# Performance work log

Hardware: AMD Instinct MI355X
Metric: run time of the kernel (lower is better)

The kernel has to match this reference:

```python
import jax, jax.numpy as jnp
import numpy as np

N, E = 50000, 800000
IN, MAP, H, O = 256, 64, 4, 64
LEAKY_SLOPE = 0.2


def setup_inputs() -> dict:
    key = jax.random.key(0)
    ks = jax.random.split(key, 12)
    x = jax.random.normal(ks[0], (N, IN), dtype=jnp.float32)
    src = jax.random.randint(ks[1], (E,), 0, N, dtype=jnp.int32)
    dst = jax.random.randint(ks[2], (E,), 0, N, dtype=jnp.int32)
    s = 1.0 / np.sqrt(IN)
    W_gat = jax.random.normal(ks[3], (IN, H * O), dtype=jnp.float32) * s
    attn_l = jax.random.normal(ks[4], (H, O), dtype=jnp.float32) * 0.1
    attn_r = jax.random.normal(ks[5], (H, O), dtype=jnp.float32) * 0.1
    gate_m_W = jax.random.normal(ks[6], (IN, MAP), dtype=jnp.float32) * s
    gate_m_b = jnp.zeros((MAP,), dtype=jnp.float32)
    gate_fn_W = jax.random.normal(ks[7], (2 * IN + MAP, H), dtype=jnp.float32) * (1.0 / np.sqrt(2 * IN + MAP))
    gate_fn_b = jnp.zeros((H,), dtype=jnp.float32)
    merge_W = jax.random.normal(ks[8], (IN + O, O), dtype=jnp.float32) * (1.0 / np.sqrt(IN + O))
    merge_b = jnp.zeros((O,), dtype=jnp.float32)
    return {"x": x, "src": src, "dst": dst, "W_gat": W_gat, "attn_l": attn_l,
            "attn_r": attn_r, "gate_m_W": gate_m_W, "gate_m_b": gate_m_b,
            "gate_fn_W": gate_fn_W, "gate_fn_b": gate_fn_b,
            "merge_W": merge_W, "merge_b": merge_b}


def _forward(x, src, dst, W_gat, attn_l, attn_r, gate_m_W, gate_m_b,
             gate_fn_W, gate_fn_b, merge_W, merge_b):
    n = x.shape[0]
    # --- gate branch: gspmm mean of x, gspmm max of linear_z over in-neighbors ---
    deg = jax.ops.segment_sum(jnp.ones_like(dst, dtype=x.dtype), dst, num_segments=n)
    mean_z = jax.ops.segment_sum(x[src], dst, num_segments=n) / jnp.maximum(deg, 1.0)[:, None]
    z = x @ gate_m_W + gate_m_b  # [N, MAP]
    max_z = jax.ops.segment_max(z[src], dst, num_segments=n)
    max_z = jnp.where(deg[:, None] > 0, max_z, 0.0)  # empty neighborhoods -> 0
    nft = jnp.concatenate([x, max_z, mean_z], axis=1)  # [N, 2*IN+MAP]
    gate = jax.nn.sigmoid(nft @ gate_fn_W + gate_fn_b)  # [N, H]
    # --- GATConv ---
    feat = (x @ W_gat).reshape(n, H, O)  # [N, H, O]
    el = jnp.einsum('nho,ho->nh', feat, attn_l)
    er = jnp.einsum('nho,ho->nh', feat, attn_r)
    e = jax.nn.leaky_relu(el[src] + er[dst], negative_slope=LEAKY_SLOPE)  # [E, H]
    m = jax.ops.segment_max(e, dst, num_segments=n)  # [N, H]
    m = jnp.where(jnp.isfinite(m), m, 0.0)
    ex = jnp.exp(e - m[dst])  # [E, H]
    s = jax.ops.segment_sum(ex, dst, num_segments=n)  # [N, H]
    alpha = ex / jnp.maximum(s[dst], 1e-16)  # [E, H]
    attn_out = jax.ops.segment_sum(feat[src] * alpha[:, :, None], dst, num_segments=n)  # [N, H, O]
    # --- gated merge ---
    gated = (gate[:, :, None] * attn_out).mean(axis=1)  # [N, O]
    merge = jnp.concatenate([x, gated], axis=1) @ merge_W + merge_b  # [N, O]
    return merge


def reference(x, src, dst, W_gat, attn_l, attn_r, gate_m_W, gate_m_b,
              gate_fn_W, gate_fn_b, merge_W, merge_b):
    return _forward(x, src, dst, W_gat, attn_l, attn_r, gate_m_W, gate_m_b,
                    gate_fn_W, gate_fn_b, merge_W, merge_b)
```

## Files before the change

kernel.cpp:

```cpp
#include <hip/hip_runtime.h>
#include <math.h>

#define NN 50000
#define NE 800000
#define LEAKY 0.2f
#define NT 26
#define CAP 96
#define NBT (8 * NT * 64)
#define BT_BLKS 54
#define GEMM_BLKS 782
#define SCAT_BLKS 3125
#define FUSE_BLKS 3907

typedef short bf16x8 __attribute__((ext_vector_type(8)));
typedef float f32x4 __attribute__((ext_vector_type(4)));
typedef float f32x2 __attribute__((ext_vector_type(2)));

__device__ __forceinline__ unsigned short f2bf(float f) {
  unsigned u = __float_as_uint(f);
  u += 0x7fffu + ((u >> 16) & 1u);
  return (unsigned short)(u >> 16);
}
__device__ __forceinline__ float leaky(float v) { return v > 0.0f ? v : LEAKY * v; }
__device__ __forceinline__ float rlf(float v, int l) {
  return __uint_as_float(__builtin_amdgcn_readlane(__float_as_uint(v), l));
}
__device__ __forceinline__ int rli(int v, int l) {
  return __builtin_amdgcn_readlane(v, l);
}

__device__ __forceinline__ bf16x8 ld_a_bf16(const float* p) {
  float4 fa = *(const float4*)p;
  float4 fb = *(const float4*)(p + 4);
  unsigned r0, r1, r2, r3;
  asm("v_cvt_pk_bf16_f32 %0, %1, %2" : "=v"(r0) : "v"(fa.x), "v"(fa.y));
  asm("v_cvt_pk_bf16_f32 %0, %1, %2" : "=v"(r1) : "v"(fa.z), "v"(fa.w));
  asm("v_cvt_pk_bf16_f32 %0, %1, %2" : "=v"(r2) : "v"(fb.x), "v"(fb.y));
  asm("v_cvt_pk_bf16_f32 %0, %1, %2" : "=v"(r3) : "v"(fb.z), "v"(fb.w));
  union { uint4 u; bf16x8 v; } c;
  c.u = make_uint4(r0, r1, r2, r3);
  return c.v;
}

#if defined(__has_builtin)
#if __has_builtin(__builtin_amdgcn_cvt_pk_f32_fp8) && \
    __has_builtin(__builtin_amdgcn_cvt_pk_fp8_f32) && \
    __has_builtin(__builtin_amdgcn_cvt_f32_fp8)
#define FP8_HW 1
#endif
#endif

#ifdef FP8_HW
__device__ __forceinline__ unsigned char f2fp8(float v) {
  return (unsigned char)(__builtin_amdgcn_cvt_pk_fp8_f32(v, v, 0u, false) & 0xFF);
}
__device__ __forceinline__ f32x2 fp8x2_lo(unsigned int v) {
  return __builtin_amdgcn_cvt_pk_f32_fp8(v, false);
}
__device__ __forceinline__ f32x2 fp8x2_hi(unsigned int v) {
  return __builtin_amdgcn_cvt_pk_f32_fp8(v, true);
}
__device__ __forceinline__ float fp8one(unsigned int v) {
  return __builtin_amdgcn_cvt_f32_fp8(v, 0);
}
#else
__device__ __forceinline__ unsigned char f2fp8(float f) {
  unsigned u = __float_as_uint(f);
  unsigned s = (u >> 31) << 7;
  unsigned a = u & 0x7FFFFFFFu;
  if (a >= 0x43E00000u) return (unsigned char)(s | 0x7E);
  if (a < 0x3C800000u) {
    float m = __uint_as_float(a) * 512.0f;
    int q = (int)(m + 0.5f); if (q > 7) q = 7;
    return (unsigned char)(s | q);
  }
  a += 0x7FFFFu + ((a >> 20) & 1);
  unsigned e = ((a >> 23) & 0xFF) - 120;
  if (e > 15) return (unsigned char)(s | 0x7E);
  return (unsigned char)(s | (e << 3) | ((a >> 20) & 7));
}
__device__ __forceinline__ float fp8dec1(unsigned b) {
  unsigned s = (b & 0x80u) << 24;
  unsigned em = b & 0x7Fu;
  unsigned e4 = em >> 3, m3 = em & 7;
  float v = e4 ? __uint_as_float(((e4 + 120) << 23) | (m3 << 20))
               : (float)m3 * 0.001953125f;
  return __uint_as_float(__float_as_uint(v) ^ s);
}
__device__ __forceinline__ f32x2 fp8x2_lo(unsigned int v) {
  f32x2 r; r[0] = fp8dec1(v & 0xFF); r[1] = fp8dec1((v >> 8) & 0xFF); return r;
}
__device__ __forceinline__ f32x2 fp8x2_hi(unsigned int v) {
  f32x2 r; r[0] = fp8dec1((v >> 16) & 0xFF); r[1] = fp8dec1((v >> 24) & 0xFF); return r;
}
__device__ __forceinline__ float fp8one(unsigned int v) { return fp8dec1(v & 0xFF); }
#endif

__device__ __forceinline__ float panel_w(int col, int k,
    const float* W_gat, const float* gate_m_W, const float* merge_W,
    const float* gate_fn_W) {
  if (col < 256)      return W_gat[k * 256 + (col & 3) * 64 + (col >> 2)];
  else if (col < 320) return gate_m_W[k * 64 + (col - 256)];
  else if (col < 384) return merge_W[k * 64 + (col - 320)];
  else if (col < 388) return gate_fn_W[k * 4 + (col - 384)];
  else if (col < 392) return gate_fn_W[(320 + k) * 4 + (col - 388)];
  return 0.0f;
}

__global__ __launch_bounds__(256) void k_prep(
    const float* __restrict__ W_gat, const float* __restrict__ gate_m_W,
    const float* __restrict__ merge_W, const float* __restrict__ gate_fn_W,
    unsigned short* __restrict__ Btf, unsigned short* __restrict__ mWf,
    unsigned char* __restrict__ zq, float* __restrict__ epay,
    unsigned char* __restrict__ featq) {
  int b = blockIdx.x, tid = threadIdx.x;
  int idx = b * 256 + tid;
  if (idx < NBT) {
    int kq = idx / (NT * 64);
    int rem = idx - kq * (NT * 64);
    int t = rem >> 6, lane = rem & 63;
    int col = t * 16 + (lane & 15);
    int k = kq * 32 + (lane >> 4) * 8;
    unsigned short* o = Btf + (size_t)idx * 8;
#pragma unroll
    for (int i = 0; i < 8; ++i)
      o[i] = f2bf(panel_w(col, k + i, W_gat, gate_m_W, merge_W, gate_fn_W));
  } else if (idx < NBT + 512) {
    int idx2 = idx - NBT;
    int kq = idx2 >> 8;
    int rem = idx2 & 255;
    int t = rem >> 6, lane = rem & 63;
    int col = t * 16 + (lane & 15);
    int k = kq * 32 + ((lane >> 4) & 3) * 8;
    unsigned short* o = mWf + (size_t)idx2 * 8;
#pragma unroll
    for (int i = 0; i < 8; ++i)
      o[i] = f2bf(merge_W[(size_t)(256 + k + i) * 64 + col]);
  } else if (b == BT_BLKS) {
    if (tid < 64) zq[(size_t)NN * 64 + tid] = 0xFE;
    if (tid < 8) epay[(size_t)NN * 8 + tid] = 0.0f;
    featq[(size_t)NN * 256 + tid] = 0;
  }
}

__global__ __launch_bounds__(256, 2) void k_gemm_scatter(
    const float* __restrict__ x, const unsigned short* __restrict__ Btf,
    const float* __restrict__ gate_m_b,
    const float* __restrict__ attn_l, const float* __restrict__ attn_r,
    unsigned char* __restrict__ featq, unsigned char* __restrict__ zq,
    float* __restrict__ xm, float* __restrict__ gx, float* __restrict__ epay,
    float* __restrict__ erv,
    const int* __restrict__ src, const int* __restrict__ dst,
    int* __restrict__ cursor, unsigned short* __restrict__ csr_src) {
  __shared__ float els[64][4][2];
  __shared__ float ers[64][4][2];
  int bq = blockIdx.x / 5, br = blockIdx.x % 5;
  if (br != 0) {
    int sIdx = bq * 4 + (br - 1);
    int e = sIdx * 256 + threadIdx.x;
    if (e < NE) {
      int n = dst[e];
      int pos = atomicAdd(&cursor[n], 1);
      if (pos < CAP) csr_src[n * CAP + pos] = (unsigned short)src[e];
    }
    return;
  }
  int lane = threadIdx.x & 63;
  int wave = threadIdx.x >> 6;
  int rowHalf = wave >> 1, colHalf = wave & 1;
  int rowB = bq * 64;
  int row0 = rowB + rowHalf * 32;
  int t0 = colHalf * 13;
  int m = lane & 15, kg = lane >> 4;
  f32x4 zero = {0.f, 0.f, 0.f, 0.f};
  f32x4 acc[2][13];
#pragma unroll
  for (int g = 0; g < 2; ++g)
#pragma unroll
    for (int t = 0; t < 13; ++t) acc[g][t] = zero;

  int r0i = row0 + m;
  int r1i = r0i + 16;
  if (r0i >= NN) r0i = NN - 1;
  if (r1i >= NN) r1i = NN - 1;
  const float* aP0 = x + (size_t)r0i * 256 + kg * 8;
  const float* aP1 = x + (size_t)r1i * 256 + kg * 8;
  const unsigned short* bB = Btf + (size_t)(t0 * 64 + lane) * 8;

  bf16x8 aC0, aC1, aN0, aN1, bC[13], bN[13];
  aC0 = ld_a_bf16(aP0);
  aC1 = ld_a_bf16(aP1);
#pragma unroll
  for (int t = 0; t < 13; ++t)
    bC[t] = *(const bf16x8*)(bB + (size_t)t * 512);
#pragma unroll 1
  for (int kq = 0; kq < 8; kq += 2) {
    aN0 = ld_a_bf16(aP0 + (kq + 1) * 32);
    aN1 = ld_a_bf16(aP1 + (kq + 1) * 32);
#pragma unroll
    for (int t = 0; t < 13; ++t)
      bN[t] = *(const bf16x8*)(bB + ((size_t)(kq + 1) * NT + t) * 512);
#pragma unroll
    for (int t = 0; t < 13; ++t)
      acc[0][t] = __builtin_amdgcn_mfma_f32_16x16x32_bf16(aC0, bC[t], acc[0][t], 0, 0, 0);
#pragma unroll
    for (int t = 0; t < 13; ++t)
      acc[1][t] = __builtin_amdgcn_mfma_f32_16x16x32_bf16(aC1, bC[t], acc[1][t], 0, 0, 0);
    int kq2 = kq + 2 < 8 ? kq + 2 : 7;
    aC0 = ld_a_bf16(aP0 + kq2 * 32);
    aC1 = ld_a_bf16(aP1 + kq2 * 32);
#pragma unroll
    for (int t = 0; t < 13; ++t)
      bC[t] = *(const bf16x8*)(bB + ((size_t)kq2 * NT + t) * 512);
#pragma unroll
    for (int t = 0; t < 13; ++t)
      acc[0][t] = __builtin_amdgcn_mfma_f32_16x16x32_bf16(aN0, bN[t], acc[0][t], 0, 0, 0);
#pragma unroll
    for (int t = 0; t < 13; ++t)
      acc[1][t] = __builtin_amdgcn_mfma_f32_16x16x32_bf16(aN1, bN[t], acc[1][t], 0, 0, 0);
  }

  int h = m & 3, od = m >> 2;
  float elp[2][4] = {{0,0,0,0},{0,0,0,0}}, erp[2][4] = {{0,0,0,0},{0,0,0,0}};
#pragma unroll
  for (int t = 0; t < 13; ++t) {
    if ((t0 + t) * 16 < 256) {
      int o = (t0 + t) * 4 + od;
      float al = attn_l[h * 64 + o];
      float ar = attn_r[h * 64 + o];
#pragma unroll
      for (int g = 0; g < 2; ++g)
#pragma unroll
        for (int r = 0; r < 4; ++r) {
          elp[g][r] += acc[g][t][r] * al;
          erp[g][r] += acc[g][t][r] * ar;
        }
    }
  }
#pragma unroll
  for (int g = 0; g < 2; ++g)
#pragma unroll
    for (int r = 0; r < 4; ++r) {
      elp[g][r] += __shfl_xor(elp[g][r], 4, 64); elp[g][r] += __shfl_xor(elp[g][r], 8, 64);
      erp[g][r] += __shfl_xor(erp[g][r], 4, 64); erp[g][r] += __shfl_xor(erp[g][r], 8, 64);
    }
  if (m < 4) {
#pragma unroll
    for (int g = 0; g < 2; ++g)
#pragma unroll
      for (int r = 0; r < 4; ++r) {
        els[rowHalf * 32 + g * 16 + kg * 4 + r][m][colHalf] = elp[g][r];
        ers[rowHalf * 32 + g * 16 + kg * 4 + r][m][colHalf] = erp[g][r];
      }
  }

#pragma unroll
  for (int g = 0; g < 2; ++g) {
    if (colHalf == 0) {
#pragma unroll
      for (int r = 0; r < 4; ++r) {
        int row = row0 + g * 16 + kg * 4 + r;
        if (row >= NN) continue;
#pragma unroll
        for (int t = 0; t < 13; ++t)
          featq[(size_t)row * 256 + t * 16 + m] = f2fp8(acc[g][t][r]);
      }
    } else {
#pragma unroll
      for (int r = 0; r < 4; ++r) {
        int row = row0 + g * 16 + kg * 4 + r;
        if (row >= NN) continue;
#pragma unroll
        for (int t = 0; t < 3; ++t)
          featq[(size_t)row * 256 + 208 + t * 16 + m] = f2fp8(acc[g][t][r]);
#pragma unroll
        for (int t = 3; t < 7; ++t) {
          int cc = (t - 3) * 16 + m;
          zq[(size_t)row * 64 + cc] = f2fp8(acc[g][t][r] + gate_m_b[cc]);
        }
#pragma unroll
        for (int t = 7; t < 11; ++t)
          xm[(size_t)row * 64 + (t - 7) * 16 + m] = acc[g][t][r];
        if (m < 4) gx[(size_t)row * 4 + m] = acc[g][11][r];
        else if (m < 8) epay[(size_t)row * 8 + (m - 4) * 2 + 1] = acc[g][11][r];
      }
    }
  }
  __syncthreads();
  int tid = threadIdx.x;
  {
    int rr = tid >> 2, h2 = tid & 3;
    int row = rowB + rr;
    if (row < NN) {
      epay[(size_t)row * 8 + h2 * 2] = els[rr][h2][0] + els[rr][h2][1];
      erv[(size_t)row * 4 + h2] = ers[rr][h2][0] + ers[rr][h2][1];
    }
  }
}

__global__ __launch_bounds__(256) void k_node(
    const unsigned char* __restrict__ zq, const unsigned char* __restrict__ featq,
    const float* __restrict__ epay, const float* __restrict__ er,
    const float* __restrict__ gx,
    const int* __restrict__ cursor, const unsigned short* __restrict__ csr_src,
    const float* __restrict__ gate_fn_W, const float* __restrict__ gate_fn_b,
    const unsigned short* __restrict__ mWf, const float* __restrict__ xm,
    const float* __restrict__ merge_b, float* __restrict__ out) {
  __shared__ float WzT[4][64];
  __shared__ float pbuf[4][16][4];
  __shared__ unsigned short gLDS[16][72];
  int tid = threadIdx.x;
  {
    int c = tid >> 2, h = tid & 3;
    WzT[h][c] = gate_fn_W[(256 + c) * 4 + h];
  }
  __syncthreads();

  int lane = tid & 63, wave = tid >> 6;
  int hh = lane >> 4, le = lane & 15;
  int rowbase = blockIdx.x * 16;
  int nodeBase = rowbase + wave * 4;
#pragma unroll 1
  for (int i = 0; i < 4; ++i) {
    int node = nodeBase + i;
    int deg = cursor[node]; if (deg > CAP) deg = CAP;
    float gated = 0.0f;
    if (deg > 0) {
      int rs = node * CAP, re = rs + deg;
      float er_h = er[(size_t)node * 4 + hh];
      f32x2 A01 = {0.f, 0.f}, A23 = {0.f, 0.f};
      float psum = 0, usum = 0;
      float mz = -INFINITY;
      int jj = rs + le;
      int s_l = (jj < re) ? (int)csr_src[jj] : NN;
#pragma unroll 1
      for (int j0 = rs; j0 < re; j0 += 16) {
        int jn = j0 + 16 + le;
        int s_nx = (jn < re) ? (int)csr_src[jn] : NN;
        bool valid = (j0 + le) < re;
        float2 eu = *(const float2*)(epay + ((size_t)(unsigned)s_l << 3) + hh * 2);
        float p = valid ? __expf(leaky(eu.x + er_h)) : 0.0f;
        psum += p;
        usum += eu.y;
        pbuf[wave][le][hh] = p;
        unsigned int fvr[16];
        unsigned int zvr[16];
#pragma unroll
        for (int e2 = 0; e2 < 16; ++e2) {
          int s = rli(s_l, e2);
          fvr[e2] = *(const unsigned int*)(featq + ((size_t)(unsigned)s << 8) + lane * 4);
        }
#pragma unroll
        for (int e2 = 0; e2 < 16; ++e2) {
          int s = rli(s_l, e2);
          zvr[e2] = zq[((size_t)(unsigned)s << 6) + lane];
        }
#pragma unroll
        for (int e2 = 0; e2 < 16; ++e2) {
          float4 pv = *(const float4*)pbuf[wave][e2];
          f32x2 p01 = {pv.x, pv.y};
          f32x2 p23 = {pv.z, pv.w};
          A01 += p01 * fp8x2_lo(fvr[e2]);
          A23 += p23 * fp8x2_hi(fvr[e2]);
          mz = fmaxf(mz, fp8one(zvr[e2]));
        }
        s_l = s_nx;
      }
#pragma unroll
      for (int off = 1; off < 16; off <<= 1) {
        psum += __shfl_xor(psum, off, 64);
        usum += __shfl_xor(usum, off, 64);
      }
      float s0 = rlf(psum, 0),  s1 = rlf(psum, 16);
      float s2 = rlf(psum, 32), s3 = rlf(psum, 48);
      float su0 = rlf(usum, 0),  su1 = rlf(usum, 16);
      float su2 = rlf(usum, 32), su3 = rlf(usum, 48);

      float g[4];
#pragma unroll
      for (int h = 0; h < 4; ++h) {
        float t = mz * WzT[h][lane];
#pragma unroll
        for (int off = 32; off; off >>= 1) t += __shfl_xor(t, off, 64);
        g[h] = t;
      }
      float inv_deg = 1.0f / (float)deg;
      float4 gx4 = *(const float4*)(gx + (size_t)node * 4);
      float g0 = 1.0f / (1.0f + __expf(-(g[0] + gx4.x + su0 * inv_deg + gate_fn_b[0])));
      float g1 = 1.0f / (1.0f + __expf(-(g[1] + gx4.y + su1 * inv_deg + gate_fn_b[1])));
      float g2 = 1.0f / (1.0f + __expf(-(g[2] + gx4.z + su2 * inv_deg + gate_fn_b[2])));
      float g3 = 1.0f / (1.0f + __expf(-(g[3] + gx4.w + su3 * inv_deg + gate_fn_b[3])));
      gated = 0.25f * (g0 * A01[0] / s0 + g1 * A01[1] / s1 +
                       g2 * A23[0] / s2 + g3 * A23[1] / s3);
    }
    gLDS[wave * 4 + i][lane] = f2bf(gated);
  }
  __syncthreads();

  int m = lane & 15, kg = lane >> 4;
  f32x4 acc = {0.f, 0.f, 0.f, 0.f};
#pragma unroll
  for (int kq = 0; kq < 2; ++kq) {
    bf16x8 a = *(const bf16x8*)(&gLDS[m][kq * 32 + kg * 8]);
    bf16x8 b = *(const bf16x8*)(mWf + (((size_t)kq * 4 + wave) * 64 + lane) * 8);
    acc = __builtin_amdgcn_mfma_f32_16x16x32_bf16(a, b, acc, 0, 0, 0);
  }
  int c = wave * 16 + m;
  float mb = merge_b[c];
#pragma unroll
  for (int r = 0; r < 4; ++r) {
    int row = rowbase + kg * 4 + r;
    out[(size_t)row * 64 + c] = acc[r] + xm[(size_t)row * 64 + c] + mb;
  }
}

extern "C" void kernel_launch(void* const* d_in, const int* in_sizes, int n_in,
                              void* d_out, int out_size, void* d_ws, size_t ws_size,
                              hipStream_t stream) {
  const float* x         = (const float*)d_in[0];
  const int*   src       = (const int*)d_in[1];
  const int*   dst       = (const int*)d_in[2];
  const float* W_gat     = (const float*)d_in[3];
  const float* attn_l    = (const float*)d_in[4];
  const float* attn_r    = (const float*)d_in[5];
  const float* gate_m_W  = (const float*)d_in[6];
  const float* gate_m_b  = (const float*)d_in[7];
  const float* gate_fn_W = (const float*)d_in[8];
  const float* gate_fn_b = (const float*)d_in[9];
  const float* merge_W   = (const float*)d_in[10];
  const float* merge_b   = (const float*)d_in[11];
  float* out = (float*)d_out;

  char* ws = (char*)d_ws;
  size_t off = 0;
  auto alloc = [&](size_t bytes) -> void* {
    off = (off + 255) & ~(size_t)255;
    void* p = ws + off;
    off += bytes;
    return p;
  };
  int* cursor    = (int*)alloc((size_t)NN * 4);
  unsigned short* csr_src = (unsigned short*)alloc((size_t)NN * CAP * 2);
  float* epay = (float*)alloc((size_t)(NN + 1) * 8 * 4);
  float* er   = (float*)alloc((size_t)NN * 4 * 4);
  float* gx   = (float*)alloc((size_t)NN * 4 * 4);
  float* xm   = (float*)alloc((size_t)NN * 64 * 4);
  unsigned char* zq    = (unsigned char*)alloc((size_t)(NN + 1) * 64);
  unsigned char* featq = (unsigned char*)alloc((size_t)(NN + 1) * 256);
  unsigned short* Btf    = (unsigned short*)alloc((size_t)NBT * 8 * 2);
  unsigned short* mWf    = (unsigned short*)alloc((size_t)512 * 8 * 2);

  hipMemsetAsync(cursor, 0, (size_t)NN * 4, stream);
  k_prep<<<BT_BLKS + 1, 256, 0, stream>>>(W_gat, gate_m_W, merge_W, gate_fn_W,
                                          Btf, mWf, zq, epay, featq);
  k_gemm_scatter<<<FUSE_BLKS, 256, 0, stream>>>(x, Btf, gate_m_b, attn_l, attn_r,
                                                featq, zq, xm, gx, epay, er,
                                                src, dst, cursor, csr_src);
  k_node<<<NN / 16, 256, 0, stream>>>(zq, featq, epay, er, gx, cursor, csr_src,
                                      gate_fn_W, gate_fn_b, mWf, xm, merge_b, out);
}
```

Measured before the change: 244.7 us.

## Fold attention vectors into GEMM panel, stage B in LDS, drop memset

Precomputes W_gat·attn_l and W_gat·attn_r as extra weight columns, so el/er come out of the MFMA GEMM instead of a post-GEMM reduction with shuffles and LDS. The GEMM is restructured so each block covers one 64-row by 13-tile column half, with B panels double-buffered in LDS through global_load_lds and occupancy raised to 3 blocks per CU. The scatter work is interleaved 2:1 with GEMM blocks. The cursor memset is folded into the prep kernel to remove one launch. The trade-off is that each x row is now read and converted twice (once per column half), and el/er are computed from bf16-rounded folded weights, which changes precision.

```diff
diff --git a/kernel.cpp b/kernel.cpp
--- a/kernel.cpp
+++ b/kernel.cpp
@@ -7,10 +7,8 @@
 #define NT 26
 #define CAP 96
 #define NBT (8 * NT * 64)
-#define BT_BLKS 54
-#define GEMM_BLKS 782
-#define SCAT_BLKS 3125
-#define FUSE_BLKS 3907
+#define PREP_BLKS 251
+#define FUSE_BLKS 4692
 
 typedef short bf16x8 __attribute__((ext_vector_type(8)));
 typedef float f32x4 __attribute__((ext_vector_type(4)));
@@ -29,9 +27,7 @@
   return __builtin_amdgcn_readlane(v, l);
 }
 
-__device__ __forceinline__ bf16x8 ld_a_bf16(const float* p) {
-  float4 fa = *(const float4*)p;
-  float4 fb = *(const float4*)(p + 4);
+__device__ __forceinline__ bf16x8 cvt8(float4 fa, float4 fb) {
   unsigned r0, r1, r2, r3;
   asm("v_cvt_pk_bf16_f32 %0, %1, %2" : "=v"(r0) : "v"(fa.x), "v"(fa.y));
   asm("v_cvt_pk_bf16_f32 %0, %1, %2" : "=v"(r1) : "v"(fa.z), "v"(fa.w));
@@ -98,65 +94,79 @@
 
 __device__ __forceinline__ float panel_w(int col, int k,
     const float* W_gat, const float* gate_m_W, const float* merge_W,
-    const float* gate_fn_W) {
+    const float* gate_fn_W, const float* attn_l, const float* attn_r) {
   if (col < 256)      return W_gat[k * 256 + (col & 3) * 64 + (col >> 2)];
   else if (col < 320) return gate_m_W[k * 64 + (col - 256)];
   else if (col < 384) return merge_W[k * 64 + (col - 320)];
   else if (col < 388) return gate_fn_W[k * 4 + (col - 384)];
   else if (col < 392) return gate_fn_W[(320 + k) * 4 + (col - 388)];
+  else if (col < 396) {
+    int h = col - 392; float s = 0.0f;
+    for (int o = 0; o < 64; ++o) s += W_gat[k * 256 + h * 64 + o] * attn_l[h * 64 + o];
+    return s;
+  } else if (col < 400) {
+    int h = col - 396; float s = 0.0f;
+    for (int o = 0; o < 64; ++o) s += W_gat[k * 256 + h * 64 + o] * attn_r[h * 64 + o];
+    return s;
+  }
   return 0.0f;
 }
 
 __global__ __launch_bounds__(256) void k_prep(
     const float* __restrict__ W_gat, const float* __restrict__ gate_m_W,
     const float* __restrict__ merge_W, const float* __restrict__ gate_fn_W,
+    const float* __restrict__ attn_l, const float* __restrict__ attn_r,
     unsigned short* __restrict__ Btf, unsigned short* __restrict__ mWf,
     unsigned char* __restrict__ zq, float* __restrict__ epay,
-    unsigned char* __restrict__ featq) {
+    unsigned char* __restrict__ featq, int* __restrict__ cursor) {
   int b = blockIdx.x, tid = threadIdx.x;
-  int idx = b * 256 + tid;
-  if (idx < NBT) {
-    int kq = idx / (NT * 64);
-    int rem = idx - kq * (NT * 64);
-    int t = rem >> 6, lane = rem & 63;
-    int col = t * 16 + (lane & 15);
-    int k = kq * 32 + (lane >> 4) * 8;
-    unsigned short* o = Btf + (size_t)idx * 8;
-#pragma unroll
-    for (int i = 0; i < 8; ++i)
-      o[i] = f2bf(panel_w(col, k + i, W_gat, gate_m_W, merge_W, gate_fn_W));
-  } else if (idx < NBT + 512) {
-    int idx2 = idx - NBT;
-    int kq = idx2 >> 8;
-    int rem = idx2 & 255;
-    int t = rem >> 6, lane = rem & 63;
-    int col = t * 16 + (lane & 15);
-    int k = kq * 32 + ((lane >> 4) & 3) * 8;
-    unsigned short* o = mWf + (size_t)idx2 * 8;
-#pragma unroll
-    for (int i = 0; i < 8; ++i)
-      o[i] = f2bf(merge_W[(size_t)(256 + k + i) * 64 + col]);
-  } else if (b == BT_BLKS) {
+  if (b < 54) {
+    int idx = b * 256 + tid;
+    if (idx < NBT) {
+      int kq = idx / (NT * 64);
+      int rem = idx - kq * (NT * 64);
+      int t = rem >> 6, lane = rem & 63;
+      int col = t * 16 + (lane & 15);
+      int k = kq * 32 + (lane >> 4) * 8;
+      unsigned short* o = Btf + (size_t)idx * 8;
+#pragma unroll
+      for (int i = 0; i < 8; ++i)
+        o[i] = f2bf(panel_w(col, k + i, W_gat, gate_m_W, merge_W, gate_fn_W,
+                            attn_l, attn_r));
+    } else {
+      int idx2 = idx - NBT;
+      int kq = idx2 >> 8;
+      int rem = idx2 & 255;
+      int t = rem >> 6, lane = rem & 63;
+      int col = t * 16 + (lane & 15);
+      int k = kq * 32 + ((lane >> 4) & 3) * 8;
+      unsigned short* o = mWf + (size_t)idx2 * 8;
+#pragma unroll
+      for (int i = 0; i < 8; ++i)
+        o[i] = f2bf(merge_W[(size_t)(256 + k + i) * 64 + col]);
+    }
+  } else if (b == 54) {
     if (tid < 64) zq[(size_t)NN * 64 + tid] = 0xFE;
     if (tid < 8) epay[(size_t)NN * 8 + tid] = 0.0f;
     featq[(size_t)NN * 256 + tid] = 0;
-  }
-}
-
-__global__ __launch_bounds__(256, 2) void k_gemm_scatter(
+  } else {
+    int i = (b - 55) * 256 + tid;
+    if (i < NN) cursor[i] = 0;
+  }
+}
+
+__global__ __launch_bounds__(256, 3) void k_gemm_scatter(
     const float* __restrict__ x, const unsigned short* __restrict__ Btf,
     const float* __restrict__ gate_m_b,
-    const float* __restrict__ attn_l, const float* __restrict__ attn_r,
     unsigned char* __restrict__ featq, unsigned char* __restrict__ zq,
     float* __restrict__ xm, float* __restrict__ gx, float* __restrict__ epay,
     float* __restrict__ erv,
     const int* __restrict__ src, const int* __restrict__ dst,
     int* __restrict__ cursor, unsigned short* __restrict__ csr_src) {
-  __shared__ float els[64][4][2];
-  __shared__ float ers[64][4][2];
-  int bq = blockIdx.x / 5, br = blockIdx.x % 5;
+  __shared__ unsigned short ldsB[2][13][64][8];
+  int bq = blockIdx.x / 3, br = blockIdx.x % 3;
   if (br != 0) {
-    int sIdx = bq * 4 + (br - 1);
+    int sIdx = bq * 2 + (br - 1);
     int e = sIdx * 256 + threadIdx.x;
     if (e < NE) {
       int n = dst[e];
@@ -165,135 +175,85 @@
     }
     return;
   }
-  int lane = threadIdx.x & 63;
-  int wave = threadIdx.x >> 6;
-  int rowHalf = wave >> 1, colHalf = wave & 1;
-  int rowB = bq * 64;
-  int row0 = rowB + rowHalf * 32;
-  int t0 = colHalf * 13;
+  int rb = bq >> 1, ch = bq & 1;
+  int lane = threadIdx.x & 63, wave = threadIdx.x >> 6;
   int m = lane & 15, kg = lane >> 4;
+  int rowB = rb * 64;
+  int t0 = ch * 13;
+  int arow = rowB + wave * 16 + m;
+  if (arow >= NN) arow = NN - 1;
+  const float* aP = x + (size_t)arow * 256 + kg * 8;
+
+  f32x4 acc[13];
   f32x4 zero = {0.f, 0.f, 0.f, 0.f};
-  f32x4 acc[2][13];
-#pragma unroll
-  for (int g = 0; g < 2; ++g)
-#pragma unroll
-    for (int t = 0; t < 13; ++t) acc[g][t] = zero;
-
-  int r0i = row0 + m;
-  int r1i = r0i + 16;
-  if (r0i >= NN) r0i = NN - 1;
-  if (r1i >= NN) r1i = NN - 1;
-  const float* aP0 = x + (size_t)r0i * 256 + kg * 8;
-  const float* aP1 = x + (size_t)r1i * 256 + kg * 8;
-  const unsigned short* bB = Btf + (size_t)(t0 * 64 + lane) * 8;
-
-  bf16x8 aC0, aC1, aN0, aN1, bC[13], bN[13];
-  aC0 = ld_a_bf16(aP0);
-  aC1 = ld_a_bf16(aP1);
-#pragma unroll
-  for (int t = 0; t < 13; ++t)
-    bC[t] = *(const bf16x8*)(bB + (size_t)t * 512);
+#pragma unroll
+  for (int t = 0; t < 13; ++t) acc[t] = zero;
+
+  for (int t = wave; t < 13; t += 4)
+    __builtin_amdgcn_global_load_lds(
+        (const __attribute__((address_space(1))) unsigned int*)
+            (Btf + ((size_t)(t0 + t)) * 512 + lane * 8),
+        (__attribute__((address_space(3))) unsigned int*)(&ldsB[0][t][0][0]),
+        16, 0, 0);
+  float4 fa = *(const float4*)aP;
+  float4 fb = *(const float4*)(aP + 4);
+  __syncthreads();
+
 #pragma unroll 1
-  for (int kq = 0; kq < 8; kq += 2) {
-    aN0 = ld_a_bf16(aP0 + (kq + 1) * 32);
-    aN1 = ld_a_bf16(aP1 + (kq + 1) * 32);
-#pragma unroll
-    for (int t = 0; t < 13; ++t)
-      bN[t] = *(const bf16x8*)(bB + ((size_t)(kq + 1) * NT + t) * 512);
-#pragma unroll
-    for (int t = 0; t < 13; ++t)
-      acc[0][t] = __builtin_amdgcn_mfma_f32_16x16x32_bf16(aC0, bC[t], acc[0][t], 0, 0, 0);
-#pragma unroll
-    for (int t = 0; t < 13; ++t)
-      acc[1][t] = __builtin_amdgcn_mfma_f32_16x16x32_bf16(aC1, bC[t], acc[1][t], 0, 0, 0);
-    int kq2 = kq + 2 < 8 ? kq + 2 : 7;
-    aC0 = ld_a_bf16(aP0 + kq2 * 32);
-    aC1 = ld_a_bf16(aP1 + kq2 * 32);
-#pragma unroll
-    for (int t = 0; t < 13; ++t)
-      bC[t] = *(const bf16x8*)(bB + ((size_t)kq2 * NT + t) * 512);
-#pragma unroll
-    for (int t = 0; t < 13; ++t)
-      acc[0][t] = __builtin_amdgcn_mfma_f32_16x16x32_bf16(aN0, bN[t], acc[0][t], 0, 0, 0);
-#pragma unroll
-    for (int t = 0; t < 13; ++t)
-      acc[1][t] = __builtin_amdgcn_mfma_f32_16x16x32_bf16(aN1, bN[t], acc[1][t], 0, 0, 0);
-  }
-
-  int h = m & 3, od = m >> 2;
-  float elp[2][4] = {{0,0,0,0},{0,0,0,0}}, erp[2][4] = {{0,0,0,0},{0,0,0,0}};
-#pragma unroll
-  for (int t = 0; t < 13; ++t) {
-    if ((t0 + t) * 16 < 256) {
-      int o = (t0 + t) * 4 + od;
-      float al = attn_l[h * 64 + o];
-      float ar = attn_r[h * 64 + o];
-#pragma unroll
-      for (int g = 0; g < 2; ++g)
-#pragma unroll
-        for (int r = 0; r < 4; ++r) {
-          elp[g][r] += acc[g][t][r] * al;
-          erp[g][r] += acc[g][t][r] * ar;
-        }
-    }
-  }
-#pragma unroll
-  for (int g = 0; g < 2; ++g)
+  for (int kq = 0; kq < 8; ++kq) {
+    int cur = kq & 1;
+    int kqn = kq < 7 ? kq + 1 : 7;
+    float4 fa_n = *(const float4*)(aP + kqn * 32);
+    float4 fb_n = *(const float4*)(aP + kqn * 32 + 4);
+    if (kq < 7) {
+      for (int t = wave; t < 13; t += 4)
+        __builtin_amdgcn_global_load_lds(
+            (const __attribute__((address_space(1))) unsigned int*)
+                (Btf + ((size_t)(kq + 1) * NT + t0 + t) * 512 + lane * 8),
+            (__attribute__((address_space(3))) unsigned int*)
+                (&ldsB[cur ^ 1][t][0][0]),
+            16, 0, 0);
+    }
+    bf16x8 a = cvt8(fa, fb);
+#pragma unroll
+    for (int t = 0; t < 13; ++t) {
+      bf16x8 bfr = *(const bf16x8*)&ldsB[cur][t][lane][0];
+      acc[t] = __builtin_amdgcn_mfma_f32_16x16x32_bf16(a, bfr, acc[t], 0, 0, 0);
+    }
+    fa = fa_n; fb = fb_n;
+    __syncthreads();
+  }
+
+  if (ch == 0) {
 #pragma unroll
     for (int r = 0; r < 4; ++r) {
-      elp[g][r] += __shfl_xor(elp[g][r], 4, 64); elp[g][r] += __shfl_xor(elp[g][r], 8, 64);
-      erp[g][r] += __shfl_xor(erp[g][r], 4, 64); erp[g][r] += __shfl_xor(erp[g][r], 8, 64);
-    }
-  if (m < 4) {
-#pragma unroll
-    for (int g = 0; g < 2; ++g)
-#pragma unroll
-      for (int r = 0; r < 4; ++r) {
-        els[rowHalf * 32 + g * 16 + kg * 4 + r][m][colHalf] = elp[g][r];
-        ers[rowHalf * 32 + g * 16 + kg * 4 + r][m][colHalf] = erp[g][r];
+      int row = rowB + wave * 16 + kg * 4 + r;
+      if (row >= NN) continue;
+#pragma unroll
+      for (int t = 0; t < 13; ++t)
+        featq[(size_t)row * 256 + t * 16 + m] = f2fp8(acc[t][r]);
+    }
+  } else {
+#pragma unroll
+    for (int r = 0; r < 4; ++r) {
+      int row = rowB + wave * 16 + kg * 4 + r;
+      if (row >= NN) continue;
+#pragma unroll
+      for (int t = 0; t < 3; ++t)
+        featq[(size_t)row * 256 + 208 + t * 16 + m] = f2fp8(acc[t][r]);
+#pragma unroll
+      for (int t = 3; t < 7; ++t) {
+        int cc = (t - 3) * 16 + m;
+        zq[(size_t)row * 64 + cc] = f2fp8(acc[t][r] + gate_m_b[cc]);
       }
-  }
-
-#pragma unroll
-  for (int g = 0; g < 2; ++g) {
-    if (colHalf == 0) {
-#pragma unroll
-      for (int r = 0; r < 4; ++r) {
-        int row = row0 + g * 16 + kg * 4 + r;
-        if (row >= NN) continue;
-#pragma unroll
-        for (int t = 0; t < 13; ++t)
-          featq[(size_t)row * 256 + t * 16 + m] = f2fp8(acc[g][t][r]);
-      }
-    } else {
-#pragma unroll
-      for (int r = 0; r < 4; ++r) {
-        int row = row0 + g * 16 + kg * 4 + r;
-        if (row >= NN) continue;
-#pragma unroll
-        for (int t = 0; t < 3; ++t)
-          featq[(size_t)row * 256 + 208 + t * 16 + m] = f2fp8(acc[g][t][r]);
-#pragma unroll
-        for (int t = 3; t < 7; ++t) {
-          int cc = (t - 3) * 16 + m;
-          zq[(size_t)row * 64 + cc] = f2fp8(acc[g][t][r] + gate_m_b[cc]);
-        }
-#pragma unroll
-        for (int t = 7; t < 11; ++t)
-          xm[(size_t)row * 64 + (t - 7) * 16 + m] = acc[g][t][r];
-        if (m < 4) gx[(size_t)row * 4 + m] = acc[g][11][r];
-        else if (m < 8) epay[(size_t)row * 8 + (m - 4) * 2 + 1] = acc[g][11][r];
-      }
-    }
-  }
-  __syncthreads();
-  int tid = threadIdx.x;
-  {
-    int rr = tid >> 2, h2 = tid & 3;
-    int row = rowB + rr;
-    if (row < NN) {
-      epay[(size_t)row * 8 + h2 * 2] = els[rr][h2][0] + els[rr][h2][1];
-      erv[(size_t)row * 4 + h2] = ers[rr][h2][0] + ers[rr][h2][1];
+#pragma unroll
+      for (int t = 7; t < 11; ++t)
+        xm[(size_t)row * 64 + (t - 7) * 16 + m] = acc[t][r];
+      float v = acc[11][r];
+      if (m < 4)       gx[(size_t)row * 4 + m] = v;
+      else if (m < 8)  epay[(size_t)row * 8 + (m - 4) * 2 + 1] = v;
+      else if (m < 12) epay[(size_t)row * 8 + (m - 8) * 2] = v;
+      else             erv[(size_t)row * 4 + (m - 12)] = v;
     }
   }
 }
@@ -450,10 +410,10 @@
   unsigned short* Btf    = (unsigned short*)alloc((size_t)NBT * 8 * 2);
   unsigned short* mWf    = (unsigned short*)alloc((size_t)512 * 8 * 2);
 
-  hipMemsetAsync(cursor, 0, (size_t)NN * 4, stream);
-  k_prep<<<BT_BLKS + 1, 256, 0, stream>>>(W_gat, gate_m_W, merge_W, gate_fn_W,
-                                          Btf, mWf, zq, epay, featq);
-  k_gemm_scatter<<<FUSE_BLKS, 256, 0, stream>>>(x, Btf, gate_m_b, attn_l, attn_r,
+  k_prep<<<PREP_BLKS, 256, 0, stream>>>(W_gat, gate_m_W, merge_W, gate_fn_W,
+                                        attn_l, attn_r, Btf, mWf, zq, epay,
+                                        featq, cursor);
+  k_gemm_scatter<<<FUSE_BLKS, 256, 0, stream>>>(x, Btf, gate_m_b,
                                                 featq, zq, xm, gx, epay, er,
                                                 src, dst, cursor, csr_src);
   k_node<<<NN / 16, 256, 0, stream>>>(zq, featq, epay, er, gx, cursor, csr_src,
```

Result: slower. 253.1 us (+3.4%).
